# Kernel optimization log

Hardware: AMD Instinct MI355X
Metric: run time of the kernel (lower is better)

The kernel has to match this reference:

```python
import jax, jax.numpy as jnp
import numpy as np

# fixed 9 neighborhood offsets (center + 8 directions), in pixel units
BASE = np.array([[0,0],[-1,-1],[0,-1],[1,-1],[-1,0],[1,0],[-1,1],[0,1],[1,1]], dtype=np.float32)
MAX_DELTA = 0.5 / 512.0


def bilinear_sample(vm, gx, gy):
    """vm: (D,H,W); gx,gy: (N,) normalized grid coords in [-1,1].
    Bilinear, padding_mode='zeros', align_corners=True. Returns (D,N)."""
    D, H, W = vm.shape
    ix = (gx + 1.0) * 0.5 * (W - 1)
    iy = (gy + 1.0) * 0.5 * (H - 1)
    x0 = jnp.floor(ix); y0 = jnp.floor(iy)
    x1 = x0 + 1.0;      y1 = y0 + 1.0
    wx1 = ix - x0; wx0 = 1.0 - wx1
    wy1 = iy - y0; wy0 = 1.0 - wy1
    fm = vm.reshape(D, H * W)

    def corner(xf, yf, wx, wy):
        valid = (xf >= 0) & (xf <= W - 1) & (yf >= 0) & (yf <= H - 1)
        xi = jnp.clip(xf.astype(jnp.int32), 0, W - 1)
        yi = jnp.clip(yf.astype(jnp.int32), 0, H - 1)
        v = jnp.take(fm, yi * W + xi, axis=1)  # (D,N) gather
        w = jnp.where(valid, wx * wy, 0.0)
        return v * w

    return (corner(x0, y0, wx0, wy0) + corner(x1, y0, wx1, wy0)
            + corner(x0, y1, wx0, wy1) + corner(x1, y1, wx1, wy1))


def setup_inputs() -> dict:
    key = jax.random.key(0)
    ks = jax.random.split(key, 5)
    B, C, Hf, Wf = 4, 256, 128, 128
    T, D = 16384, 128
    fmap = jax.random.normal(ks[0], (B, C, Hf, Wf), dtype=jnp.float32)
    coords = jax.random.uniform(ks[1], (B, T, 2), dtype=jnp.float32)
    W_proj = jax.random.normal(ks[2], (D, C), dtype=jnp.float32) * (1.0 / np.sqrt(C))
    W1 = jax.random.normal(ks[3], (D, D), dtype=jnp.float32) * (1.0 / np.sqrt(D))
    b1 = jnp.zeros((D,), dtype=jnp.float32)
    W2 = jax.random.normal(ks[4], (2, D), dtype=jnp.float32) * (1.0 / np.sqrt(D))
    b2 = jnp.zeros((2,), dtype=jnp.float32)
    return {"fmap": fmap, "coords": coords, "W_proj": W_proj,
            "W1": W1, "b1": b1, "W2": W2, "b2": b2}


def reference(fmap, coords, W_proj, W1, b1, W2, b2):
    B, C, Hf, Wf = fmap.shape
    T = coords.shape[1]
    K = BASE.shape[0]
    # 1x1 conv projection
    vm = jnp.einsum('bchw,dc->bdhw', fmap, W_proj)  # (B,D,Hf,Wf)
    # offsets: one pixel step in [0,1] coords (align_corners=True)
    step = jnp.array([1.0 / (Wf - 1), 1.0 / (Hf - 1)], dtype=coords.dtype)
    grid = coords[:, :, None, :] + jnp.asarray(BASE)[None, None] * step  # (B,T,K,2)
    grid = grid * 2.0 - 1.0                                            # normalize to [-1,1]
    grid = grid.reshape(B, T * K, 2)
    feat = jax.vmap(bilinear_sample)(vm, grid[..., 0], grid[..., 1])   # (B,D,T*K)
    D = feat.shape[1]
    feat = feat.transpose(0, 2, 1).reshape(B, T, K, D).mean(axis=2)    # (B,T,D)
    h = jax.nn.relu(feat @ W1.T + b1)
    delta = jnp.tanh(h @ W2.T + b2) * MAX_DELTA
    return coords + delta
```

## Files before the change

kernel.cpp:

```cpp
#include <hip/hip_runtime.h>
#include <cstddef>

#define NB 4
#define NC 256
#define ND 128
#define NH 128
#define NW 128
#define NHW (NH*NW)
#define NT 16384

typedef short   short8  __attribute__((ext_vector_type(8)));
typedef unsigned short ushort8 __attribute__((ext_vector_type(8)));
typedef float   floatx4 __attribute__((ext_vector_type(4)));
typedef float   floatx2 __attribute__((ext_vector_type(2)));

__device__ __forceinline__ unsigned pk_bf16(float a, float b) {
    unsigned ua = __float_as_uint(a);
    unsigned ub = __float_as_uint(b);
    ua += 0x7fffu + ((ua >> 16) & 1u);
    ub += 0x7fffu + ((ub >> 16) & 1u);
    return (ua >> 16) | (ub & 0xffff0000u);
}

__device__ __forceinline__ float bf2f(unsigned short u) {
    return __uint_as_float(((unsigned)u) << 16);
}

__device__ __forceinline__ unsigned fp8x4_from_f32(float v0, float v1, float v2, float v3) {
#if __has_builtin(__builtin_amdgcn_cvt_pk_fp8_f32)
    int r = 0;
    r = __builtin_amdgcn_cvt_pk_fp8_f32(v0, v1, r, false);
    r = __builtin_amdgcn_cvt_pk_fp8_f32(v2, v3, r, true);
    return (unsigned)r;
#else
    auto enc1 = [](float x) -> unsigned {
        unsigned u = __float_as_uint(x);
        unsigned s = (u >> 24) & 0x80u;
        float ax = fabsf(x);
        if (ax < 0.015625f) return s;
        if (ax > 448.f) return s | 0x7Eu;
        u = __float_as_uint(ax);
        u += 0x7ffffu + ((u >> 20) & 1u);
        unsigned e = (u >> 23) - 120u;
        return s | ((e & 15u) << 3) | ((u >> 20) & 7u);
    };
    return enc1(v0) | (enc1(v1) << 8) | (enc1(v2) << 16) | (enc1(v3) << 24);
#endif
}

template <bool HI>
__device__ __forceinline__ floatx2 fp8x2_to_f32(unsigned w) {
#if __has_builtin(__builtin_amdgcn_cvt_pk_f32_fp8)
    return __builtin_amdgcn_cvt_pk_f32_fp8((int)w, HI);
#else
    auto dec1 = [](unsigned b) -> float {
        unsigned s = (b & 0x80u) << 24;
        unsigned em = b & 0x7Fu;
        if (em == 0) return __uint_as_float(s);
        return __uint_as_float(s | (((em >> 3) + 120u) << 23) | ((em & 7u) << 20));
    };
    unsigned v = HI ? (w >> 16) : w;
    floatx2 r; r.x = dec1(v & 0xFFu); r.y = dec1((v >> 8) & 0xFFu);
    return r;
#endif
}

__global__ __launch_bounds__(512, 4)
void proj_kernel(const float* __restrict__ fmap, const float* __restrict__ Wp,
                 const float* __restrict__ W1, unsigned char* __restrict__ vm,
                 float* __restrict__ W1T)
{
    const int bi = blockIdx.x;
    if (bi >= 512) {
        if (bi == 512)
            for (int i = threadIdx.x; i < ND*ND; i += 512)
                W1T[(i & 127)*ND + (i >> 7)] = W1[i];
        return;
    }
    __shared__ unsigned short awp[8*8*64*8];

    const int t    = threadIdx.x;
    const int lane = t & 63;
    const int w    = t >> 6;
    const int l15  = lane & 15;
    const int q    = lane >> 4;
    const int cq   = q * 8;

    {
        const int dt = w;
        const float* wr0 = Wp + (size_t)(dt*16 + l15)*NC + cq;
        #pragma unroll
        for (int ch = 0; ch < 8; ++ch) {
            float4 g0 = *(const float4*)(wr0 + ch*32);
            float4 g1 = *(const float4*)(wr0 + ch*32 + 4);
            uint4 pk = make_uint4(pk_bf16(g0.x,g0.y), pk_bf16(g0.z,g0.w),
                                  pk_bf16(g1.x,g1.y), pk_bf16(g1.z,g1.w));
            *(uint4*)&awp[((dt*8 + ch)*64 + lane)*8] = pk;
        }
    }
    __syncthreads();

    const int b    = (bi & 7) >> 1;
    const int slot = ((bi >> 3) << 1) | (bi & 1);
    const int p    = slot*128 + w*16 + l15;

    floatx4 acc[8];
    #pragma unroll
    for (int i = 0; i < 8; ++i) acc[i] = (floatx4)(0.f);

    const float* fbase = fmap + (size_t)b*NC*NHW + p;

    #pragma unroll 2
    for (int c0 = 0; c0 < 8; ++c0) {
        const float* bp = fbase + (size_t)(c0*32 + cq)*NHW;
        float f[8];
        #pragma unroll
        for (int j = 0; j < 8; ++j) f[j] = bp[(size_t)j*NHW];
        union { short8 v; unsigned u[4]; } bc;
        #pragma unroll
        for (int j = 0; j < 4; ++j) bc.u[j] = pk_bf16(f[2*j], f[2*j+1]);
        #pragma unroll
        for (int dt = 0; dt < 8; ++dt) {
            short8 afr = *(const short8*)&awp[((dt*8 + c0)*64 + lane)*8];
            acc[dt] = __builtin_amdgcn_mfma_f32_16x16x32_bf16(afr, bc.v, acc[dt], 0, 0, 0);
        }
    }
    unsigned char* vrow = vm + ((size_t)(b*NHW + p))*ND;
    #pragma unroll
    for (int dt = 0; dt < 8; ++dt) {
        floatx4 v = acc[dt];
        *(unsigned*)&vrow[dt*16 + q*4] = fp8x4_from_f32(v[0], v[1], v[2], v[3]);
    }
}

__global__ __launch_bounds__(512, 8)
void gather_mlp(const unsigned char* __restrict__ vm, const float* __restrict__ coords,
                const float* __restrict__ W1T, const float* __restrict__ b1,
                const float* __restrict__ W2, const float* __restrict__ b2,
                float* __restrict__ out)
{
    __shared__ unsigned short feat[64 * 136];
    __shared__ float part[64][17];
    const int t  = threadIdx.x;
    const int bi = blockIdx.x;
    const int b  = (bi & 7) >> 1;
    const int s  = ((bi >> 3) << 1) | (bi & 1);
    const int g0 = b * NT + s * 64;

    {
        const int pt = t >> 3;
        const int c8 = t & 7;
        const int g  = g0 + pt;
        const float cx = coords[(size_t)g*2 + 0];
        const float cy = coords[(size_t)g*2 + 1];
        const float ix = cx * (float)(NW - 1);
        const float iy = cy * (float)(NH - 1);
        const float x0f = floorf(ix), y0f = floorf(iy);
        const int x0 = (int)x0f, y0 = (int)y0f;
        const float wx1 = ix - x0f, wy1 = iy - y0f;
        const float wxv[4] = {1.f - wx1, 1.f, 1.f, wx1};
        const float wyv[4] = {1.f - wy1, 1.f, 1.f, wy1};
        floatx2 acc[8];
        #pragma unroll
        for (int k = 0; k < 8; ++k) acc[k] = (floatx2)(0.f);
        const unsigned char* vmb = vm + (size_t)b*NHW*ND + c8*16;
        #pragma unroll
        for (int j = 0; j < 4; ++j) {
            const int Y  = y0 - 1 + j;
            const int Yc = min(max(Y, 0), NH-1);
            const bool vy = (Y >= 0) & (Y < NH);
            #pragma unroll
            for (int i = 0; i < 4; ++i) {
                const int X  = x0 - 1 + i;
                const int Xc = min(max(X, 0), NW-1);
                const bool vx = (X >= 0) & (X < NW);
                const float wgt = (vx & vy) ? wxv[i]*wyv[j] : 0.f;
                uint4 u = *(const uint4*)(vmb + (size_t)(Yc*NW + Xc)*ND);
                const floatx2 w2 = {wgt, wgt};
                acc[0] += w2 * fp8x2_to_f32<false>(u.x);
                acc[1] += w2 * fp8x2_to_f32<true >(u.x);
                acc[2] += w2 * fp8x2_to_f32<false>(u.y);
                acc[3] += w2 * fp8x2_to_f32<true >(u.y);
                acc[4] += w2 * fp8x2_to_f32<false>(u.z);
                acc[5] += w2 * fp8x2_to_f32<true >(u.z);
                acc[6] += w2 * fp8x2_to_f32<false>(u.w);
                acc[7] += w2 * fp8x2_to_f32<true >(u.w);
            }
        }
        const float s9 = 1.f/9.f;
        unsigned pk[8];
        #pragma unroll
        for (int k = 0; k < 8; ++k)
            pk[k] = pk_bf16(acc[k].x*s9, acc[k].y*s9);
        *(uint4*)&feat[pt*136 + c8*16]     = make_uint4(pk[0],pk[1],pk[2],pk[3]);
        *(uint4*)&feat[pt*136 + c8*16 + 8] = make_uint4(pk[4],pk[5],pk[6],pk[7]);
    }
    __syncthreads();

    {
        const int pt = t & 63;
        const int eb = t >> 6;
        const int e0 = __builtin_amdgcn_readfirstlane(eb * 16);
        floatx2 acc[8];
        #pragma unroll
        for (int k = 0; k < 8; ++k) acc[k] = *(const floatx2*)&b1[e0 + 2*k];
        #pragma unroll 2
        for (int d = 0; d < ND; d += 8) {
            ushort8 u = *(const ushort8*)&feat[pt*136 + d];
            #pragma unroll
            for (int jj = 0; jj < 8; ++jj) {
                const float fv = bf2f(u[jj]);
                const floatx2 f2 = {fv, fv};
                const float* wrow = W1T + (size_t)(d + jj)*ND + e0;
                #pragma unroll
                for (int k = 0; k < 8; ++k)
                    acc[k] += f2 * (*(const floatx2*)&wrow[2*k]);
            }
        }
        float s0 = 0.f, s1 = 0.f;
        const float* w20 = W2 + e0;
        const float* w21 = W2 + ND + e0;
        #pragma unroll
        for (int k = 0; k < 8; ++k) {
            float h0 = fmaxf(acc[k].x, 0.f);
            float h1 = fmaxf(acc[k].y, 0.f);
            s0 = fmaf(h0, w20[2*k], fmaf(h1, w20[2*k+1], s0));
            s1 = fmaf(h0, w21[2*k], fmaf(h1, w21[2*k+1], s1));
        }
        part[pt][eb*2 + 0] = s0;
        part[pt][eb*2 + 1] = s1;
    }
    __syncthreads();

    if (t < 64) {
        const int g = g0 + t;
        float s0 = 0.f, s1 = 0.f;
        #pragma unroll
        for (int k = 0; k < 8; ++k) { s0 += part[t][2*k]; s1 += part[t][2*k+1]; }
        const float cx = coords[(size_t)g*2 + 0];
        const float cy = coords[(size_t)g*2 + 1];
        const float MD = 0.5f / 512.0f;
        float2 o = make_float2(cx + tanhf(s0 + b2[0]) * MD,
                               cy + tanhf(s1 + b2[1]) * MD);
        *(float2*)&out[(size_t)g*2] = o;
    }
}

extern "C" void kernel_launch(void* const* d_in, const int* in_sizes, int n_in,
                              void* d_out, int out_size, void* d_ws, size_t ws_size,
                              hipStream_t stream)
{
    const float* fmap   = (const float*)d_in[0];
    const float* coords = (const float*)d_in[1];
    const float* Wp     = (const float*)d_in[2];
    const float* W1     = (const float*)d_in[3];
    const float* b1     = (const float*)d_in[4];
    const float* W2     = (const float*)d_in[5];
    const float* b2     = (const float*)d_in[6];
    float* out = (float*)d_out;

    unsigned char* vm = (unsigned char*)d_ws;
    float* W1T = (float*)((char*)d_ws + (size_t)NB*NHW*ND);

    proj_kernel<<<dim3(512 + 1), 512, 0, stream>>>(fmap, Wp, W1, vm, W1T);
    gather_mlp<<<dim3(1024), 512, 0, stream>>>(vm, coords, W1T, b1, W2, b2, out);
}
```

Baseline: 159.5 us.

## Bucket query points spatially via counting sort before gather-MLP for cache locality

Adds histogram, scan and scatter kernels that bin the query points into 8x8-pixel spatial buckets per batch. The gather-MLP kernel then runs one block per bucket, in 64-point chunks, so neighbouring samples reuse the same projected feature rows from cache. This is meant to cut scattered gather traffic. In exchange it adds four small serial launches, atomics, and load imbalance, because bucket sizes vary and the occupancy hint drops from 8 to 4. The projection loop is also fully unrolled, and the W1 transpose moves into the prep kernel.

Measured after the change: 217.2 us. 36.2% more time.

```diff
diff --git a/kernel.cpp b/kernel.cpp
--- a/kernel.cpp
+++ b/kernel.cpp
@@ -8,6 +8,7 @@
 #define NW 128
 #define NHW (NH*NW)
 #define NT 16384
+#define NBKT 1024
 
 typedef short   short8  __attribute__((ext_vector_type(8)));
 typedef unsigned short ushort8 __attribute__((ext_vector_type(8)));
@@ -27,56 +28,77 @@
 }
 
 __device__ __forceinline__ unsigned fp8x4_from_f32(float v0, float v1, float v2, float v3) {
-#if __has_builtin(__builtin_amdgcn_cvt_pk_fp8_f32)
     int r = 0;
     r = __builtin_amdgcn_cvt_pk_fp8_f32(v0, v1, r, false);
     r = __builtin_amdgcn_cvt_pk_fp8_f32(v2, v3, r, true);
     return (unsigned)r;
-#else
-    auto enc1 = [](float x) -> unsigned {
-        unsigned u = __float_as_uint(x);
-        unsigned s = (u >> 24) & 0x80u;
-        float ax = fabsf(x);
-        if (ax < 0.015625f) return s;
-        if (ax > 448.f) return s | 0x7Eu;
-        u = __float_as_uint(ax);
-        u += 0x7ffffu + ((u >> 20) & 1u);
-        unsigned e = (u >> 23) - 120u;
-        return s | ((e & 15u) << 3) | ((u >> 20) & 7u);
-    };
-    return enc1(v0) | (enc1(v1) << 8) | (enc1(v2) << 16) | (enc1(v3) << 24);
-#endif
-}
-
+}
 template <bool HI>
 __device__ __forceinline__ floatx2 fp8x2_to_f32(unsigned w) {
-#if __has_builtin(__builtin_amdgcn_cvt_pk_f32_fp8)
     return __builtin_amdgcn_cvt_pk_f32_fp8((int)w, HI);
-#else
-    auto dec1 = [](unsigned b) -> float {
-        unsigned s = (b & 0x80u) << 24;
-        unsigned em = b & 0x7Fu;
-        if (em == 0) return __uint_as_float(s);
-        return __uint_as_float(s | (((em >> 3) + 120u) << 23) | ((em & 7u) << 20));
-    };
-    unsigned v = HI ? (w >> 16) : w;
-    floatx2 r; r.x = dec1(v & 0xFFu); r.y = dec1((v >> 8) & 0xFFu);
-    return r;
-#endif
+}
+
+__device__ __forceinline__ int bucket_of(float cx, float cy, int b) {
+    int x0 = (int)floorf(cx * (float)(NW - 1));
+    int y0 = (int)floorf(cy * (float)(NH - 1));
+    x0 = min(max(x0, 0), NW - 1);
+    y0 = min(max(y0, 0), NH - 1);
+    return b * 256 + (y0 >> 3) * 16 + (x0 >> 3);
+}
+
+__global__ void prep_kernel(const float* __restrict__ W1, float* __restrict__ W1T,
+                            int* __restrict__ counts, int* __restrict__ cursor)
+{
+    const int t = threadIdx.x;
+    counts[t] = 0;
+    cursor[t] = 0;
+    for (int i = t; i < ND*ND; i += 1024)
+        W1T[(i & 127)*ND + (i >> 7)] = W1[i];
+}
+
+__global__ __launch_bounds__(1024)
+void hist_kernel(const float* __restrict__ coords, int* __restrict__ counts)
+{
+    const int g = blockIdx.x * 1024 + threadIdx.x;
+    const float cx = coords[(size_t)g*2 + 0];
+    const float cy = coords[(size_t)g*2 + 1];
+    atomicAdd(&counts[bucket_of(cx, cy, g >> 14)], 1);
+}
+
+__global__ __launch_bounds__(1024)
+void scan_kernel(const int* __restrict__ counts, int* __restrict__ starts)
+{
+    __shared__ int sd[1024];
+    const int t = threadIdx.x;
+    const int my = counts[t];
+    sd[t] = my;
+    __syncthreads();
+    for (int off = 1; off < 1024; off <<= 1) {
+        int v = (t >= off) ? sd[t - off] : 0;
+        __syncthreads();
+        sd[t] += v;
+        __syncthreads();
+    }
+    starts[t] = sd[t] - my;
+}
+
+__global__ __launch_bounds__(1024)
+void scatter_kernel(const float* __restrict__ coords, const int* __restrict__ starts,
+                    int* __restrict__ cursor, int* __restrict__ order)
+{
+    const int g = blockIdx.x * 1024 + threadIdx.x;
+    const float cx = coords[(size_t)g*2 + 0];
+    const float cy = coords[(size_t)g*2 + 1];
+    const int bkt = bucket_of(cx, cy, g >> 14);
+    const int pos = atomicAdd(&cursor[bkt], 1);
+    order[starts[bkt] + pos] = g;
 }
 
 __global__ __launch_bounds__(512, 4)
 void proj_kernel(const float* __restrict__ fmap, const float* __restrict__ Wp,
-                 const float* __restrict__ W1, unsigned char* __restrict__ vm,
-                 float* __restrict__ W1T)
+                 unsigned char* __restrict__ vm)
 {
     const int bi = blockIdx.x;
-    if (bi >= 512) {
-        if (bi == 512)
-            for (int i = threadIdx.x; i < ND*ND; i += 512)
-                W1T[(i & 127)*ND + (i >> 7)] = W1[i];
-        return;
-    }
     __shared__ unsigned short awp[8*8*64*8];
 
     const int t    = threadIdx.x;
@@ -110,7 +132,7 @@
 
     const float* fbase = fmap + (size_t)b*NC*NHW + p;
 
-    #pragma unroll 2
+    #pragma unroll
     for (int c0 = 0; c0 < 8; ++c0) {
         const float* bp = fbase + (size_t)(c0*32 + cq)*NHW;
         float f[8];
@@ -133,116 +155,130 @@
     }
 }
 
-__global__ __launch_bounds__(512, 8)
+__global__ __launch_bounds__(512, 4)
 void gather_mlp(const unsigned char* __restrict__ vm, const float* __restrict__ coords,
+                const int* __restrict__ counts, const int* __restrict__ starts,
+                const int* __restrict__ order,
                 const float* __restrict__ W1T, const float* __restrict__ b1,
                 const float* __restrict__ W2, const float* __restrict__ b2,
                 float* __restrict__ out)
 {
     __shared__ unsigned short feat[64 * 136];
     __shared__ float part[64][17];
-    const int t  = threadIdx.x;
-    const int bi = blockIdx.x;
-    const int b  = (bi & 7) >> 1;
-    const int s  = ((bi >> 3) << 1) | (bi & 1);
-    const int g0 = b * NT + s * 64;
-
-    {
-        const int pt = t >> 3;
-        const int c8 = t & 7;
-        const int g  = g0 + pt;
-        const float cx = coords[(size_t)g*2 + 0];
-        const float cy = coords[(size_t)g*2 + 1];
-        const float ix = cx * (float)(NW - 1);
-        const float iy = cy * (float)(NH - 1);
-        const float x0f = floorf(ix), y0f = floorf(iy);
-        const int x0 = (int)x0f, y0 = (int)y0f;
-        const float wx1 = ix - x0f, wy1 = iy - y0f;
-        const float wxv[4] = {1.f - wx1, 1.f, 1.f, wx1};
-        const float wyv[4] = {1.f - wy1, 1.f, 1.f, wy1};
-        floatx2 acc[8];
-        #pragma unroll
-        for (int k = 0; k < 8; ++k) acc[k] = (floatx2)(0.f);
-        const unsigned char* vmb = vm + (size_t)b*NHW*ND + c8*16;
-        #pragma unroll
-        for (int j = 0; j < 4; ++j) {
-            const int Y  = y0 - 1 + j;
-            const int Yc = min(max(Y, 0), NH-1);
-            const bool vy = (Y >= 0) & (Y < NH);
+    __shared__ int gidx[64];
+    const int t   = threadIdx.x;
+    const int bkt = blockIdx.x;
+    const int n     = counts[bkt];
+    const int start = starts[bkt];
+    const int chunks = (n + 63) >> 6;
+
+    for (int c = 0; c < chunks; ++c) {
+        const int np = min(n - c*64, 64);
+
+        {
+            const int pt = t >> 3;
+            const int c8 = t & 7;
+            if (pt < np) {
+                const int g = order[start + c*64 + pt];
+                if (c8 == 0) gidx[pt] = g;
+                const int b = g >> 14;
+                const float cx = coords[(size_t)g*2 + 0];
+                const float cy = coords[(size_t)g*2 + 1];
+                const float ix = cx * (float)(NW - 1);
+                const float iy = cy * (float)(NH - 1);
+                const float x0f = floorf(ix), y0f = floorf(iy);
+                const int x0 = (int)x0f, y0 = (int)y0f;
+                const float wx1 = ix - x0f, wy1 = iy - y0f;
+                const float wxv[4] = {1.f - wx1, 1.f, 1.f, wx1};
+                const float wyv[4] = {1.f - wy1, 1.f, 1.f, wy1};
+                floatx2 acc[8];
+                #pragma unroll
+                for (int k = 0; k < 8; ++k) acc[k] = (floatx2)(0.f);
+                const unsigned char* vmb = vm + (size_t)b*NHW*ND + c8*16;
+                #pragma unroll
+                for (int j = 0; j < 4; ++j) {
+                    const int Y  = y0 - 1 + j;
+                    const int Yc = min(max(Y, 0), NH-1);
+                    const bool vy = (Y >= 0) & (Y < NH);
+                    #pragma unroll
+                    for (int i = 0; i < 4; ++i) {
+                        const int X  = x0 - 1 + i;
+                        const int Xc = min(max(X, 0), NW-1);
+                        const bool vx = (X >= 0) & (X < NW);
+                        const float wgt = (vx & vy) ? wxv[i]*wyv[j] : 0.f;
+                        uint4 u = *(const uint4*)(vmb + (size_t)(Yc*NW + Xc)*ND);
+                        const floatx2 w2 = {wgt, wgt};
+                        acc[0] += w2 * fp8x2_to_f32<false>(u.x);
+                        acc[1] += w2 * fp8x2_to_f32<true >(u.x);
+                        acc[2] += w2 * fp8x2_to_f32<false>(u.y);
+                        acc[3] += w2 * fp8x2_to_f32<true >(u.y);
+                        acc[4] += w2 * fp8x2_to_f32<false>(u.z);
+                        acc[5] += w2 * fp8x2_to_f32<true >(u.z);
+                        acc[6] += w2 * fp8x2_to_f32<false>(u.w);
+                        acc[7] += w2 * fp8x2_to_f32<true >(u.w);
+                    }
+                }
+                const float s9 = 1.f/9.f;
+                unsigned pk[8];
+                #pragma unroll
+                for (int k = 0; k < 8; ++k)
+                    pk[k] = pk_bf16(acc[k].x*s9, acc[k].y*s9);
+                *(uint4*)&feat[pt*136 + c8*16]     = make_uint4(pk[0],pk[1],pk[2],pk[3]);
+                *(uint4*)&feat[pt*136 + c8*16 + 8] = make_uint4(pk[4],pk[5],pk[6],pk[7]);
+            }
+        }
+        __syncthreads();
+
+        {
+            const int pt = t & 63;
+            const int eb = t >> 6;
+            if (pt < np) {
+                const int e0 = __builtin_amdgcn_readfirstlane(eb * 16);
+                floatx2 acc[8];
+                #pragma unroll
+                for (int k = 0; k < 8; ++k) acc[k] = *(const floatx2*)&b1[e0 + 2*k];
+                #pragma unroll 2
+                for (int d = 0; d < ND; d += 8) {
+                    ushort8 u = *(const ushort8*)&feat[pt*136 + d];
+                    #pragma unroll
+                    for (int jj = 0; jj < 8; ++jj) {
+                        const float fv = bf2f(u[jj]);
+                        const floatx2 f2 = {fv, fv};
+                        const float* wrow = W1T + (size_t)(d + jj)*ND + e0;
+                        #pragma unroll
+                        for (int k = 0; k < 8; ++k)
+                            acc[k] += f2 * (*(const floatx2*)&wrow[2*k]);
+                    }
+                }
+                float s0 = 0.f, s1 = 0.f;
+                const float* w20 = W2 + e0;
+                const float* w21 = W2 + ND + e0;
+                #pragma unroll
+                for (int k = 0; k < 8; ++k) {
+                    float h0 = fmaxf(acc[k].x, 0.f);
+                    float h1 = fmaxf(acc[k].y, 0.f);
+                    s0 = fmaf(h0, w20[2*k], fmaf(h1, w20[2*k+1], s0));
+                    s1 = fmaf(h0, w21[2*k], fmaf(h1, w21[2*k+1], s1));
+                }
+                part[pt][eb*2 + 0] = s0;
+                part[pt][eb*2 + 1] = s1;
+            }
+        }
+        __syncthreads();
+
+        if (t < np) {
+            const int g = gidx[t];
+            float s0 = 0.f, s1 = 0.f;
             #pragma unroll
-            for (int i = 0; i < 4; ++i) {
-                const int X  = x0 - 1 + i;
-                const int Xc = min(max(X, 0), NW-1);
-                const bool vx = (X >= 0) & (X < NW);
-                const float wgt = (vx & vy) ? wxv[i]*wyv[j] : 0.f;
-                uint4 u = *(const uint4*)(vmb + (size_t)(Yc*NW + Xc)*ND);
-                const floatx2 w2 = {wgt, wgt};
-                acc[0] += w2 * fp8x2_to_f32<false>(u.x);
-                acc[1] += w2 * fp8x2_to_f32<true >(u.x);
-                acc[2] += w2 * fp8x2_to_f32<false>(u.y);
-                acc[3] += w2 * fp8x2_to_f32<true >(u.y);
-                acc[4] += w2 * fp8x2_to_f32<false>(u.z);
-                acc[5] += w2 * fp8x2_to_f32<true >(u.z);
-                acc[6] += w2 * fp8x2_to_f32<false>(u.w);
-                acc[7] += w2 * fp8x2_to_f32<true >(u.w);
-            }
-        }
-        const float s9 = 1.f/9.f;
-        unsigned pk[8];
-        #pragma unroll
-        for (int k = 0; k < 8; ++k)
-            pk[k] = pk_bf16(acc[k].x*s9, acc[k].y*s9);
-        *(uint4*)&feat[pt*136 + c8*16]     = make_uint4(pk[0],pk[1],pk[2],pk[3]);
-        *(uint4*)&feat[pt*136 + c8*16 + 8] = make_uint4(pk[4],pk[5],pk[6],pk[7]);
-    }
-    __syncthreads();
-
-    {
-        const int pt = t & 63;
-        const int eb = t >> 6;
-        const int e0 = __builtin_amdgcn_readfirstlane(eb * 16);
-        floatx2 acc[8];
-        #pragma unroll
-        for (int k = 0; k < 8; ++k) acc[k] = *(const floatx2*)&b1[e0 + 2*k];
-        #pragma unroll 2
-        for (int d = 0; d < ND; d += 8) {
-            ushort8 u = *(const ushort8*)&feat[pt*136 + d];
-            #pragma unroll
-            for (int jj = 0; jj < 8; ++jj) {
-                const float fv = bf2f(u[jj]);
-                const floatx2 f2 = {fv, fv};
-                const float* wrow = W1T + (size_t)(d + jj)*ND + e0;
-                #pragma unroll
-                for (int k = 0; k < 8; ++k)
-                    acc[k] += f2 * (*(const floatx2*)&wrow[2*k]);
-            }
-        }
-        float s0 = 0.f, s1 = 0.f;
-        const float* w20 = W2 + e0;
-        const float* w21 = W2 + ND + e0;
-        #pragma unroll
-        for (int k = 0; k < 8; ++k) {
-            float h0 = fmaxf(acc[k].x, 0.f);
-            float h1 = fmaxf(acc[k].y, 0.f);
-            s0 = fmaf(h0, w20[2*k], fmaf(h1, w20[2*k+1], s0));
-            s1 = fmaf(h0, w21[2*k], fmaf(h1, w21[2*k+1], s1));
-        }
-        part[pt][eb*2 + 0] = s0;
-        part[pt][eb*2 + 1] = s1;
-    }
-    __syncthreads();
-
-    if (t < 64) {
-        const int g = g0 + t;
-        float s0 = 0.f, s1 = 0.f;
-        #pragma unroll
-        for (int k = 0; k < 8; ++k) { s0 += part[t][2*k]; s1 += part[t][2*k+1]; }
-        const float cx = coords[(size_t)g*2 + 0];
-        const float cy = coords[(size_t)g*2 + 1];
-        const float MD = 0.5f / 512.0f;
-        float2 o = make_float2(cx + tanhf(s0 + b2[0]) * MD,
-                               cy + tanhf(s1 + b2[1]) * MD);
-        *(float2*)&out[(size_t)g*2] = o;
+            for (int k = 0; k < 8; ++k) { s0 += part[t][2*k]; s1 += part[t][2*k+1]; }
+            const float cx = coords[(size_t)g*2 + 0];
+            const float cy = coords[(size_t)g*2 + 1];
+            const float MD = 0.5f / 512.0f;
+            float2 o = make_float2(cx + tanhf(s0 + b2[0]) * MD,
+                                   cy + tanhf(s1 + b2[1]) * MD);
+            *(float2*)&out[(size_t)g*2] = o;
+        }
+        __syncthreads();
     }
 }
 
@@ -260,8 +296,18 @@
     float* out = (float*)d_out;
 
     unsigned char* vm = (unsigned char*)d_ws;
-    float* W1T = (float*)((char*)d_ws + (size_t)NB*NHW*ND);
-
-    proj_kernel<<<dim3(512 + 1), 512, 0, stream>>>(fmap, Wp, W1, vm, W1T);
-    gather_mlp<<<dim3(1024), 512, 0, stream>>>(vm, coords, W1T, b1, W2, b2, out);
-}
+    char* base = (char*)d_ws + (size_t)NB*NHW*ND;
+    float* W1T   = (float*)base;
+    int* counts  = (int*)(base + 65536);
+    int* cursor  = (int*)(base + 65536 + 4096);
+    int* starts  = (int*)(base + 65536 + 8192);
+    int* order   = (int*)(base + 65536 + 12288);
+
+    prep_kernel   <<<dim3(1),   1024, 0, stream>>>(W1, W1T, counts, cursor);
+    hist_kernel   <<<dim3(64),  1024, 0, stream>>>(coords, counts);
+    scan_kernel   <<<dim3(1),   1024, 0, stream>>>(counts, starts);
+    scatter_kernel<<<dim3(64),  1024, 0, stream>>>(coords, starts, cursor, order);
+    proj_kernel   <<<dim3(512),  512, 0, stream>>>(fmap, Wp, vm);
+    gather_mlp    <<<dim3(NBKT), 512, 0, stream>>>(vm, coords, counts, starts, order,
+                                                   W1T, b1, W2, b2, out);
+}
```
